# Performance work log

Hardware: AMD Instinct MI355X
Metric: run time of the kernel (lower is better)

Reference implementation:

```python
import jax, jax.numpy as jnp
import numpy as np

HIDDEN = 1024
HEADS = 16
HEAD_DIM = HIDDEN // HEADS


def setup_inputs() -> dict:
    key = jax.random.key(0)
    ks = jax.random.split(key, 11)
    B, S = 2, 2048
    s = 1.0 / np.sqrt(HIDDEN)
    return {
        "query": jax.random.normal(ks[0], (B, S, HIDDEN), jnp.float32),
        "key": jax.random.normal(ks[1], (B, S, HIDDEN), jnp.float32),
        "value": jax.random.normal(ks[2], (B, S, HIDDEN), jnp.float32),
        "Wq": jax.random.normal(ks[3], (HIDDEN, HIDDEN), jnp.float32) * s,
        "bq": jnp.zeros((HIDDEN,), jnp.float32),
        "Wk": jax.random.normal(ks[4], (HIDDEN, HIDDEN), jnp.float32) * s,
        "bk": jnp.zeros((HIDDEN,), jnp.float32),
        "Wv": jax.random.normal(ks[5], (HIDDEN, HIDDEN), jnp.float32) * s,
        "bv": jnp.zeros((HIDDEN,), jnp.float32),
        "Wo": jax.random.normal(ks[6], (HIDDEN, HIDDEN), jnp.float32) * s,
        "bo": jnp.zeros((HIDDEN,), jnp.float32),
    }


def reference(query, key, value, Wq, bq, Wk, bk, Wv, bv, Wo, bo):
    B, S, _ = query.shape
    # QKV projections (torch Linear: x @ W.T + b)
    Q = query @ Wq.T + bq
    K = key @ Wk.T + bk
    V = value @ Wv.T + bv
    # split heads: [B, S, H, D] -> [B, H, S, D]
    Q = Q.reshape(B, S, HEADS, HEAD_DIM).transpose(0, 2, 1, 3)
    K = K.reshape(B, S, HEADS, HEAD_DIM).transpose(0, 2, 1, 3)
    V = V.reshape(B, S, HEADS, HEAD_DIM).transpose(0, 2, 1, 3)
    scale = jnp.sqrt(jnp.float32(HEAD_DIM))
    # energy = Q K^T / sqrt(d)  -> [B, H, Sq, Sk]
    energy = jnp.einsum("bhqd,bhkd->bhqk", Q, K) / scale
    attn = jax.nn.softmax(energy, axis=-1)
    # dropout p=0.0 in eval -> identity
    x = jnp.einsum("bhqk,bhkd->bhqd", attn, V)
    x = x.transpose(0, 2, 1, 3).reshape(B, S, HIDDEN)
    return x @ Wo.T + bo
```

## Files before the change

kernel.cpp:

```cpp
#include <hip/hip_runtime.h>

typedef __attribute__((ext_vector_type(8))) short short8;
typedef __attribute__((ext_vector_type(4))) float f32x4;

#define SEQ 2048
#define NB 2
#define HID 1024
#define NH 16
#define HD 64
#define MS (NB * SEQ)

#define QSCALE 0.18033688011112042f

typedef const __attribute__((address_space(1))) unsigned int* gptr_t;
typedef __attribute__((address_space(3))) unsigned int* lptr_t;

__device__ inline ushort f2bf(float f) {
  union { float f; unsigned u; } x; x.f = f;
  unsigned r = x.u + 0x7fffu + ((x.u >> 16) & 1u);
  return (ushort)(r >> 16);
}

__device__ inline unsigned cvt_pk_bf16(float lo, float hi) {
  unsigned r;
  asm volatile("v_cvt_pk_bf16_f32 %0, %1, %2" : "=v"(r) : "v"(lo), "v"(hi));
  return r;
}

__global__ void cast3(const float* __restrict__ a, const float* __restrict__ b,
                      const float* __restrict__ c, ushort* __restrict__ oa,
                      ushort* __restrict__ ob, ushort* __restrict__ oc, int n4) {
  const int z = blockIdx.y;
  const float* in = (z == 0) ? a : (z == 1) ? b : c;
  ushort* out = (z == 0) ? oa : (z == 1) ? ob : oc;
  int i = blockIdx.x * 256 + threadIdx.x;
  if (i >= n4) return;
  float4 v = reinterpret_cast<const float4*>(in)[i];
  ushort4 o;
  o.x = f2bf(v.x); o.y = f2bf(v.y); o.z = f2bf(v.z); o.w = f2bf(v.w);
  reinterpret_cast<ushort4*>(out)[i] = o;
}

__global__ void cast4(const float* __restrict__ a, const float* __restrict__ b,
                      const float* __restrict__ c, const float* __restrict__ d,
                      ushort* __restrict__ oa, ushort* __restrict__ ob,
                      ushort* __restrict__ oc, ushort* __restrict__ od, int n4) {
  const int z = blockIdx.y;
  const float* in = (z == 0) ? a : (z == 1) ? b : (z == 2) ? c : d;
  ushort* out = (z == 0) ? oa : (z == 1) ? ob : (z == 2) ? oc : od;
  int i = blockIdx.x * 256 + threadIdx.x;
  if (i >= n4) return;
  float4 v = reinterpret_cast<const float4*>(in)[i];
  ushort4 o;
  o.x = f2bf(v.x); o.y = f2bf(v.y); o.z = f2bf(v.z); o.w = f2bf(v.w);
  reinterpret_cast<ushort4*>(out)[i] = o;
}

template <int BN, int OUT>
__device__ __forceinline__ void gemm_body(const ushort* __restrict__ A,
                                          const ushort* __restrict__ B,
                                          const float* __restrict__ bias,
                                          void* __restrict__ Out,
                                          ushort* As, ushort* Bs) {
  constexpr int NJ = BN / 32;
  const int tid = threadIdx.x;
  const int wave = tid >> 6, lane = tid & 63;
  const int lr = lane & 15, lg = lane >> 4;
  const int wr = wave >> 1, wc = wave & 1;
  const int bm = blockIdx.y, bn = blockIdx.x;

  f32x4 acc[4][NJ];
#pragma unroll
  for (int i = 0; i < 4; ++i)
#pragma unroll
    for (int j = 0; j < NJ; ++j) acc[i][j] = (f32x4)(0.f);

  const int l4 = lane >> 2;
  const int lc = (lane & 3) * 8;

  for (int k0 = 0; k0 < HID; k0 += 32) {
#pragma unroll
    for (int c = 0; c < 2; ++c) {
      const int chunk = wave * 2 + c;
      const ushort* ga = &A[(size_t)(bm * 128 + chunk * 16 + l4) * HID + k0 + lc];
      __builtin_amdgcn_global_load_lds((gptr_t)(const void*)ga, (lptr_t)(void*)&As[chunk * 512], 16, 0, 0);
    }
    if (BN == 128) {
#pragma unroll
      for (int c = 0; c < 2; ++c) {
        const int chunk = wave * 2 + c;
        const ushort* gb = &B[(size_t)(bn * BN + chunk * 16 + l4) * HID + k0 + lc];
        __builtin_amdgcn_global_load_lds((gptr_t)(const void*)gb, (lptr_t)(void*)&Bs[chunk * 512], 16, 0, 0);
      }
    } else {
      const ushort* gb = &B[(size_t)(bn * BN + wave * 16 + l4) * HID + k0 + lc];
      __builtin_amdgcn_global_load_lds((gptr_t)(const void*)gb, (lptr_t)(void*)&Bs[wave * 512], 16, 0, 0);
    }
    __syncthreads();
    short8 af[4], bf[NJ];
#pragma unroll
    for (int i = 0; i < 4; ++i)
      af[i] = *reinterpret_cast<const short8*>(&As[(wr * 64 + i * 16 + lr) * 32 + lg * 8]);
#pragma unroll
    for (int j = 0; j < NJ; ++j)
      bf[j] = *reinterpret_cast<const short8*>(&Bs[(wc * (BN / 2) + j * 16 + lr) * 32 + lg * 8]);
#pragma unroll
    for (int i = 0; i < 4; ++i)
#pragma unroll
      for (int j = 0; j < NJ; ++j)
        acc[i][j] = __builtin_amdgcn_mfma_f32_16x16x32_bf16(af[i], bf[j], acc[i][j], 0, 0, 0);
    __syncthreads();
  }

#pragma unroll
  for (int i = 0; i < 4; ++i)
#pragma unroll
    for (int j = 0; j < NJ; ++j) {
      const int row0 = bm * 128 + wr * 64 + i * 16 + lg * 4;
      const int col = bn * BN + wc * (BN / 2) + j * 16 + lr;
      const float bv = bias[col];
      if (OUT == 0) {
#pragma unroll
        for (int r = 0; r < 4; ++r)
          ((float*)Out)[(size_t)(row0 + r) * HID + col] = acc[i][j][r] + bv;
      } else if (OUT == 1) {
#pragma unroll
        for (int r = 0; r < 4; ++r)
          ((ushort*)Out)[(size_t)(row0 + r) * HID + col] = f2bf(acc[i][j][r] + bv);
      } else if (OUT == 2) {
#pragma unroll
        for (int r = 0; r < 4; ++r)
          ((ushort*)Out)[(size_t)(row0 + r) * HID + col] = f2bf((acc[i][j][r] + bv) * QSCALE);
      } else {
        uint2 w;
        w.x = cvt_pk_bf16(acc[i][j][0] + bv, acc[i][j][1] + bv);
        w.y = cvt_pk_bf16(acc[i][j][2] + bv, acc[i][j][3] + bv);
        size_t off = ((size_t)((row0 >> 11) * NH + (col >> 6)) << 17) +
                     ((size_t)(col & 63) << 11) + (size_t)(row0 & 2047);
        *reinterpret_cast<uint2*>(&((ushort*)Out)[off]) = w;
      }
    }
}

__global__ __launch_bounds__(256) void gemm_qkv(const ushort* __restrict__ A0, const ushort* __restrict__ A1,
                                                const ushort* __restrict__ A2, const ushort* __restrict__ W0,
                                                const ushort* __restrict__ W1, const ushort* __restrict__ W2,
                                                const float* __restrict__ b0, const float* __restrict__ b1,
                                                const float* __restrict__ b2, ushort* __restrict__ O0,
                                                ushort* __restrict__ O1, ushort* __restrict__ O2) {
  __shared__ alignas(16) ushort As[128 * 32];
  __shared__ alignas(16) ushort Bs[128 * 32];
  const int z = blockIdx.z;
  if (z == 0)      gemm_body<128, 2>(A0, W0, b0, O0, As, Bs);
  else if (z == 1) gemm_body<128, 1>(A1, W1, b1, O1, As, Bs);
  else             gemm_body<128, 3>(A2, W2, b2, O2, As, Bs);
}

__global__ __launch_bounds__(256) void gemm_wo(const ushort* __restrict__ A, const ushort* __restrict__ W,
                                               const float* __restrict__ bias, float* __restrict__ O) {
  __shared__ alignas(16) ushort As[128 * 32];
  __shared__ alignas(16) ushort Bs[64 * 32];
  gemm_body<64, 0>(A, W, bias, O, As, Bs);
}

__global__ __launch_bounds__(256) void attn_kernel(const ushort* __restrict__ Q,
                                                   const ushort* __restrict__ Kp,
                                                   const ushort* __restrict__ VT,
                                                   ushort* __restrict__ Op) {
  __shared__ alignas(16) ushort Ks[2 * 4096];
  __shared__ alignas(16) ushort Vs[2 * 4096];

  const int qt = blockIdx.x;
  const int bh = blockIdx.y;
  const int b = bh >> 4, h = bh & 15;
  const int tid = threadIdx.x;
  const int wave = tid >> 6;
  const int lane = tid & 63;
  const int lr = lane & 15;
  const int lg = lane >> 4;

  const size_t base = (size_t)b * SEQ * HID + h * HD;
  const size_t vtbase = (size_t)bh * HD * SEQ;

  short8 qf[2];
  const int qrow = qt * 64 + wave * 16 + lr;
#pragma unroll
  for (int kk = 0; kk < 2; ++kk)
    qf[kk] = *reinterpret_cast<const short8*>(&Q[base + (size_t)qrow * HID + kk * 32 + lg * 8]);

  f32x4 acc[4];
#pragma unroll
  for (int nd = 0; nd < 4; ++nd) acc[nd] = (f32x4)(0.f);
  float mrun = -1e30f, lrun = 0.f;

  const int rsub = lane >> 3;
  const int srcsl = ((lane & 7) ^ rsub) * 8;
  const int s0 = lr + ((lg & 1) << 5);
  const int s1v = s0 + 16;

  auto stage = [&](int buf, int kt) {
#pragma unroll
    for (int c = 0; c < 2; ++c) {
      const int chunk = wave * 2 + c;
      const int row = chunk * 8 + rsub;
      const ushort* gk = &Kp[base + (size_t)(kt * 64 + row) * HID + srcsl];
      __builtin_amdgcn_global_load_lds((gptr_t)(const void*)gk,
                                       (lptr_t)(void*)&Ks[buf * 4096 + chunk * 512], 16, 0, 0);
      const ushort* gv = &VT[vtbase + (size_t)row * SEQ + kt * 64 + srcsl];
      __builtin_amdgcn_global_load_lds((gptr_t)(const void*)gv,
                                       (lptr_t)(void*)&Vs[buf * 4096 + chunk * 512], 16, 0, 0);
    }
  };

  stage(0, 0);
  __syncthreads();

  int cur = 0;
  for (int kt = 0; kt < SEQ / 64; ++kt) {
    const int nxt = (kt + 1 < SEQ / 64) ? kt + 1 : 0;
    stage(cur ^ 1, nxt);

    const char* kb = (const char*)&Ks[cur * 4096];
    const char* vb = (const char*)&Vs[cur * 4096];

    f32x4 sa[4];
#pragma unroll
    for (int n = 0; n < 4; ++n) sa[n] = (f32x4)(0.f);
#pragma unroll
    for (int kk = 0; kk < 2; ++kk) {
      short8 kf[4];
#pragma unroll
      for (int n = 0; n < 4; ++n)
        kf[n] = *reinterpret_cast<const short8*>(
            kb + (n * 16 + lr) * 128 + ((kk * 64 + lg * 16) ^ ((lr & 7) << 4)));
#pragma unroll
      for (int n = 0; n < 4; ++n)
        sa[n] = __builtin_amdgcn_mfma_f32_16x16x32_bf16(kf[n], qf[kk], sa[n], 0, 0, 0);
    }

    float pmax = sa[0][0];
#pragma unroll
    for (int n = 0; n < 4; ++n)
#pragma unroll
      for (int r = 0; r < 4; ++r) pmax = fmaxf(pmax, sa[n][r]);
    pmax = fmaxf(pmax, __shfl_xor(pmax, 16, 64));
    pmax = fmaxf(pmax, __shfl_xor(pmax, 32, 64));
    if (__any(pmax > mrun + 8.f)) {
      const float mnew = fmaxf(mrun, pmax);
      const float corr = exp2f(mrun - mnew);
      mrun = mnew;
      lrun *= corr;
#pragma unroll
      for (int nd = 0; nd < 4; ++nd) acc[nd] *= corr;
    }
    float psum = 0.f;
#pragma unroll
    for (int n = 0; n < 4; ++n)
#pragma unroll
      for (int r = 0; r < 4; ++r) {
        float p = exp2f(sa[n][r] - mrun);
        sa[n][r] = p;
        psum += p;
      }
    psum += __shfl_xor(psum, 16, 64);
    psum += __shfl_xor(psum, 32, 64);
    lrun += psum;

    short8 vtf[4][2];
#pragma unroll
    for (int nd = 0; nd < 4; ++nd)
#pragma unroll
      for (int kk = 0; kk < 2; ++kk)
        vtf[nd][kk] = *reinterpret_cast<const short8*>(
            vb + (nd * 16 + lr) * 128 + ((kk * 64 + lg * 16) ^ ((lr & 7) << 4)));

#pragma unroll
    for (int kk = 0; kk < 2; ++kk) {
      unsigned pw0 = 0, pw1 = 0, pw2 = 0, pw3 = 0;
#pragma unroll
      for (int half = 0; half < 2; ++half) {
        const int nsel = kk * 2 + half;
        unsigned w0 = cvt_pk_bf16(sa[nsel][0], sa[nsel][1]);
        unsigned w1 = cvt_pk_bf16(sa[nsel][2], sa[nsel][3]);
        int d0 = __shfl((int)w0, s0, 64);
        int d1 = __shfl((int)w1, s0, 64);
        int d2 = __shfl((int)w0, s1v, 64);
        int d3 = __shfl((int)w1, s1v, 64);
        const bool take = ((lg >> 1) == half);
        pw0 = take ? (unsigned)d0 : pw0;
        pw1 = take ? (unsigned)d1 : pw1;
        pw2 = take ? (unsigned)d2 : pw2;
        pw3 = take ? (unsigned)d3 : pw3;
      }
      union { unsigned u[4]; short8 v; } pu;
      pu.u[0] = pw0; pu.u[1] = pw1; pu.u[2] = pw2; pu.u[3] = pw3;
#pragma unroll
      for (int nd = 0; nd < 4; ++nd)
        acc[nd] = __builtin_amdgcn_mfma_f32_16x16x32_bf16(vtf[nd][kk], pu.v, acc[nd], 0, 0, 0);
    }
    __syncthreads();
    cur ^= 1;
  }

  const float linv = 1.f / lrun;
#pragma unroll
  for (int nd = 0; nd < 4; ++nd) {
    uint2 o;
    o.x = cvt_pk_bf16(acc[nd][0] * linv, acc[nd][1] * linv);
    o.y = cvt_pk_bf16(acc[nd][2] * linv, acc[nd][3] * linv);
    *reinterpret_cast<uint2*>(&Op[base + (size_t)qrow * HID + nd * 16 + lg * 4]) = o;
  }
}

extern "C" void kernel_launch(void* const* d_in, const int* in_sizes, int n_in,
                              void* d_out, int out_size, void* d_ws, size_t ws_size,
                              hipStream_t stream) {
  const float* query = (const float*)d_in[0];
  const float* key   = (const float*)d_in[1];
  const float* value = (const float*)d_in[2];
  const float* Wq = (const float*)d_in[3];
  const float* bq = (const float*)d_in[4];
  const float* Wk = (const float*)d_in[5];
  const float* bk = (const float*)d_in[6];
  const float* Wv = (const float*)d_in[7];
  const float* bv = (const float*)d_in[8];
  const float* Wo = (const float*)d_in[9];
  const float* bo = (const float*)d_in[10];

  const size_t actElems = (size_t)MS * HID;
  const size_t wElems = (size_t)HID * HID;
  char* ws = (char*)d_ws;
  ushort* qb = (ushort*)(ws + 0);
  ushort* kb = (ushort*)(ws + actElems * 2);
  ushort* vb = (ushort*)(ws + actElems * 4);
  ushort* wq = (ushort*)(ws + actElems * 6);
  ushort* wk = (ushort*)(ws + actElems * 6 + wElems * 2);
  ushort* wv = (ushort*)(ws + actElems * 6 + wElems * 4);
  ushort* wo = (ushort*)(ws + actElems * 6 + wElems * 6);
  ushort* Qp   = (ushort*)(ws + actElems * 6 + wElems * 8);
  ushort* Kp   = (ushort*)(ws + actElems * 8 + wElems * 8);
  ushort* VTp  = (ushort*)(ws + actElems * 10 + wElems * 8);
  ushort* attn = (ushort*)(ws + actElems * 12 + wElems * 8);

  dim3 cg3((unsigned)(actElems / 4 / 256), 3);
  cast3<<<cg3, 256, 0, stream>>>(query, key, value, qb, kb, vb, (int)(actElems / 4));
  dim3 cg4((unsigned)(wElems / 4 / 256), 4);
  cast4<<<cg4, 256, 0, stream>>>(Wq, Wk, Wv, Wo, wq, wk, wv, wo, (int)(wElems / 4));

  dim3 gq(HID / 128, MS / 128, 3);
  gemm_qkv<<<gq, 256, 0, stream>>>(qb, kb, vb, wq, wk, wv, bq, bk, bv, Qp, Kp, VTp);

  dim3 ga(SEQ / 64, NB * NH);
  attn_kernel<<<ga, 256, 0, stream>>>(Qp, Kp, VTp, attn);

  dim3 go(HID / 64, MS / 128);
  gemm_wo<<<go, 256, 0, stream>>>(attn, wo, bo, (float*)d_out);
}
```

Before: 295.5 us.

## Rewrite attention with 32x32 MFMA, split-KV waves, and separate V transpose

The attention kernel now uses 512-thread blocks covering 128 query rows each. Two wave groups each process half of the key sequence, using 32x32x16 MFMA tiles and a larger shared-memory buffer, and their partial softmax states are merged through LDS at the end. The V projection GEMM now writes row-major output, and a separate transpose kernel builds V^T instead of the scattered transposed store in the GEMM epilogue. This is meant to raise MFMA efficiency and reuse of K/V tiles per block. The costs are an extra kernel launch, an extra pass over V, and more LDS per block, which may limit occupancy.

```diff
diff --git a/kernel.cpp b/kernel.cpp
--- a/kernel.cpp
+++ b/kernel.cpp
@@ -2,6 +2,7 @@
 
 typedef __attribute__((ext_vector_type(8))) short short8;
 typedef __attribute__((ext_vector_type(4))) float f32x4;
+typedef __attribute__((ext_vector_type(16))) float f32x16;
 
 #define SEQ 2048
 #define NB 2
@@ -21,9 +22,9 @@
   return (ushort)(r >> 16);
 }
 
-__device__ inline unsigned cvt_pk_bf16(float lo, float hi) {
+__device__ __forceinline__ unsigned cvt_pk_bf16(float lo, float hi) {
   unsigned r;
-  asm volatile("v_cvt_pk_bf16_f32 %0, %1, %2" : "=v"(r) : "v"(lo), "v"(hi));
+  asm("v_cvt_pk_bf16_f32 %0, %1, %2" : "=v"(r) : "v"(lo), "v"(hi));
   return r;
 }
 
@@ -119,25 +120,15 @@
       const int row0 = bm * 128 + wr * 64 + i * 16 + lg * 4;
       const int col = bn * BN + wc * (BN / 2) + j * 16 + lr;
       const float bv = bias[col];
-      if (OUT == 0) {
-#pragma unroll
-        for (int r = 0; r < 4; ++r)
-          ((float*)Out)[(size_t)(row0 + r) * HID + col] = acc[i][j][r] + bv;
-      } else if (OUT == 1) {
-#pragma unroll
-        for (int r = 0; r < 4; ++r)
-          ((ushort*)Out)[(size_t)(row0 + r) * HID + col] = f2bf(acc[i][j][r] + bv);
-      } else if (OUT == 2) {
-#pragma unroll
-        for (int r = 0; r < 4; ++r)
-          ((ushort*)Out)[(size_t)(row0 + r) * HID + col] = f2bf((acc[i][j][r] + bv) * QSCALE);
-      } else {
-        uint2 w;
-        w.x = cvt_pk_bf16(acc[i][j][0] + bv, acc[i][j][1] + bv);
-        w.y = cvt_pk_bf16(acc[i][j][2] + bv, acc[i][j][3] + bv);
-        size_t off = ((size_t)((row0 >> 11) * NH + (col >> 6)) << 17) +
-                     ((size_t)(col & 63) << 11) + (size_t)(row0 & 2047);
-        *reinterpret_cast<uint2*>(&((ushort*)Out)[off]) = w;
+#pragma unroll
+      for (int r = 0; r < 4; ++r) {
+        float v = acc[i][j][r] + bv;
+        if (OUT == 0)
+          ((float*)Out)[(size_t)(row0 + r) * HID + col] = v;
+        else if (OUT == 1)
+          ((ushort*)Out)[(size_t)(row0 + r) * HID + col] = f2bf(v);
+        else
+          ((ushort*)Out)[(size_t)(row0 + r) * HID + col] = f2bf(v * QSCALE);
       }
     }
 }
@@ -153,7 +144,7 @@
   const int z = blockIdx.z;
   if (z == 0)      gemm_body<128, 2>(A0, W0, b0, O0, As, Bs);
   else if (z == 1) gemm_body<128, 1>(A1, W1, b1, O1, As, Bs);
-  else             gemm_body<128, 3>(A2, W2, b2, O2, As, Bs);
+  else             gemm_body<128, 1>(A2, W2, b2, O2, As, Bs);
 }
 
 __global__ __launch_bounds__(256) void gemm_wo(const ushort* __restrict__ A, const ushort* __restrict__ W,
@@ -163,152 +154,231 @@
   gemm_body<64, 0>(A, W, bias, O, As, Bs);
 }
 
-__global__ __launch_bounds__(256) void attn_kernel(const ushort* __restrict__ Q,
-                                                   const ushort* __restrict__ Kp,
-                                                   const ushort* __restrict__ VT,
-                                                   ushort* __restrict__ Op) {
-  __shared__ alignas(16) ushort Ks[2 * 4096];
-  __shared__ alignas(16) ushort Vs[2 * 4096];
-
-  const int qt = blockIdx.x;
-  const int bh = blockIdx.y;
+__global__ __launch_bounds__(256) void vt_kernel(const ushort* __restrict__ Vp, ushort* __restrict__ VT) {
+  __shared__ ushort Lt[64][68];
+  const int sb = blockIdx.x, bh = blockIdx.y;
   const int b = bh >> 4, h = bh & 15;
+  const int t = threadIdx.x;
+  const int s4 = (t & 15) * 4, d4 = (t >> 4) * 4;
+  ushort v[4][4];
+#pragma unroll
+  for (int r = 0; r < 4; ++r) {
+    ushort4 x = *reinterpret_cast<const ushort4*>(
+        &Vp[(size_t)(b * SEQ + sb * 64 + s4 + r) * HID + h * 64 + d4]);
+    v[r][0] = x.x; v[r][1] = x.y; v[r][2] = x.z; v[r][3] = x.w;
+  }
+#pragma unroll
+  for (int j = 0; j < 4; ++j) {
+    ushort4 y; y.x = v[0][j]; y.y = v[1][j]; y.z = v[2][j]; y.w = v[3][j];
+    *reinterpret_cast<ushort4*>(&Lt[d4 + j][s4]) = y;
+  }
+  __syncthreads();
+  const int dl = t >> 2, s0 = (t & 3) * 16;
+  ushort4 o[4];
+#pragma unroll
+  for (int p = 0; p < 4; ++p) o[p] = *reinterpret_cast<const ushort4*>(&Lt[dl][s0 + p * 4]);
+  ushort* dst = &VT[((size_t)bh * HD + dl) * SEQ + sb * 64 + s0];
+#pragma unroll
+  for (int p = 0; p < 4; ++p) *reinterpret_cast<ushort4*>(&dst[p * 4]) = o[p];
+}
+
+__device__ __forceinline__ short8 ldfrag(const char* tb, int r, int g) {
+  return *reinterpret_cast<const short8*>(tb + r * 128 + ((g * 16) ^ ((r & 7) << 4)));
+}
+
+__global__ __launch_bounds__(512, 4) void attn_kernel(const ushort* __restrict__ Q,
+                                                      const ushort* __restrict__ Kp,
+                                                      const ushort* __restrict__ VT,
+                                                      ushort* __restrict__ Op) {
+  __shared__ alignas(16) ushort lds[32768];
+
+  const int bh = blockIdx.x;
+  const int b = bh >> 4, h = bh & 15;
+  const int qt = blockIdx.y;
   const int tid = threadIdx.x;
-  const int wave = tid >> 6;
-  const int lane = tid & 63;
-  const int lr = lane & 15;
-  const int lg = lane >> 4;
+  const int w = tid >> 6, lane = tid & 63;
+  const int q = lane & 31, hi = lane >> 5;
+  const int qsub = w & 3, chf = w >> 2;
 
   const size_t base = (size_t)b * SEQ * HID + h * HD;
   const size_t vtbase = (size_t)bh * HD * SEQ;
 
-  short8 qf[2];
-  const int qrow = qt * 64 + wave * 16 + lr;
-#pragma unroll
-  for (int kk = 0; kk < 2; ++kk)
-    qf[kk] = *reinterpret_cast<const short8*>(&Q[base + (size_t)qrow * HID + kk * 32 + lg * 8]);
-
-  f32x4 acc[4];
-#pragma unroll
-  for (int nd = 0; nd < 4; ++nd) acc[nd] = (f32x4)(0.f);
-  float mrun = -1e30f, lrun = 0.f;
-
-  const int rsub = lane >> 3;
-  const int srcsl = ((lane & 7) ^ rsub) * 8;
-  const int s0 = lr + ((lg & 1) << 5);
-  const int s1v = s0 + 16;
-
-  auto stage = [&](int buf, int kt) {
-#pragma unroll
-    for (int c = 0; c < 2; ++c) {
-      const int chunk = wave * 2 + c;
-      const int row = chunk * 8 + rsub;
-      const ushort* gk = &Kp[base + (size_t)(kt * 64 + row) * HID + srcsl];
-      __builtin_amdgcn_global_load_lds((gptr_t)(const void*)gk,
-                                       (lptr_t)(void*)&Ks[buf * 4096 + chunk * 512], 16, 0, 0);
-      const ushort* gv = &VT[vtbase + (size_t)row * SEQ + kt * 64 + srcsl];
-      __builtin_amdgcn_global_load_lds((gptr_t)(const void*)gv,
-                                       (lptr_t)(void*)&Vs[buf * 4096 + chunk * 512], 16, 0, 0);
-    }
+  const int qrow = qt * 128 + qsub * 32 + q;
+  short8 qf[4];
+#pragma unroll
+  for (int s = 0; s < 4; ++s)
+    qf[s] = *reinterpret_cast<const short8*>(&Q[base + (size_t)qrow * HID + s * 16 + hi * 8]);
+
+  f32x16 acc0 = (f32x16)(0.f), acc1 = (f32x16)(0.f);
+  float mrun = -3e38f;
+  float ps0 = 0.f, ps1 = 0.f, ps2 = 0.f, ps3 = 0.f;
+
+  const int tsel = w >> 1, part = w & 1, sh = tsel & 1;
+  const bool isK = tsel < 2;
+  const int r8 = lane >> 3;
+  const int sx = ((lane & 7) ^ r8) * 8;
+
+  auto stage = [&](int buf, int ktb) {
+    const int kt = ktb + sh * 16;
+#pragma unroll
+    for (int c = 0; c < 4; ++c) {
+      const int G = part * 4 + c, r = G * 8 + r8;
+      const ushort* src;
+      ushort* dst;
+      if (isK) {
+        src = &Kp[base + (size_t)(kt * 64 + r) * HID + sx];
+        dst = &lds[(sh * 2 + buf) * 4096 + G * 512];
+      } else {
+        src = &VT[vtbase + (size_t)r * SEQ + kt * 64 + sx];
+        dst = &lds[16384 + (sh * 2 + buf) * 4096 + G * 512];
+      }
+      __builtin_amdgcn_global_load_lds((gptr_t)(const void*)src, (lptr_t)(void*)dst, 16, 0, 0);
+    }
+  };
+
+  auto mkfrag = [&](const unsigned* Wg) -> short8 {
+    unsigned X0 = (unsigned)__shfl_xor((int)Wg[0], 32, 64);
+    unsigned X1 = (unsigned)__shfl_xor((int)Wg[1], 32, 64);
+    unsigned X2 = (unsigned)__shfl_xor((int)Wg[2], 32, 64);
+    unsigned X3 = (unsigned)__shfl_xor((int)Wg[3], 32, 64);
+    union { unsigned u[4]; short8 v; } p;
+    p.u[0] = hi ? X2 : Wg[0];
+    p.u[1] = hi ? X3 : Wg[1];
+    p.u[2] = hi ? Wg[2] : X0;
+    p.u[3] = hi ? Wg[3] : X1;
+    return p.v;
   };
 
   stage(0, 0);
   __syncthreads();
 
-  int cur = 0;
-  for (int kt = 0; kt < SEQ / 64; ++kt) {
-    const int nxt = (kt + 1 < SEQ / 64) ? kt + 1 : 0;
-    stage(cur ^ 1, nxt);
-
-    const char* kb = (const char*)&Ks[cur * 4096];
-    const char* vb = (const char*)&Vs[cur * 4096];
-
-    f32x4 sa[4];
-#pragma unroll
-    for (int n = 0; n < 4; ++n) sa[n] = (f32x4)(0.f);
-#pragma unroll
-    for (int kk = 0; kk < 2; ++kk) {
-      short8 kf[4];
-#pragma unroll
-      for (int n = 0; n < 4; ++n)
-        kf[n] = *reinterpret_cast<const short8*>(
-            kb + (n * 16 + lr) * 128 + ((kk * 64 + lg * 16) ^ ((lr & 7) << 4)));
-#pragma unroll
-      for (int n = 0; n < 4; ++n)
-        sa[n] = __builtin_amdgcn_mfma_f32_16x16x32_bf16(kf[n], qf[kk], sa[n], 0, 0, 0);
-    }
-
-    float pmax = sa[0][0];
-#pragma unroll
-    for (int n = 0; n < 4; ++n)
-#pragma unroll
-      for (int r = 0; r < 4; ++r) pmax = fmaxf(pmax, sa[n][r]);
-    pmax = fmaxf(pmax, __shfl_xor(pmax, 16, 64));
-    pmax = fmaxf(pmax, __shfl_xor(pmax, 32, 64));
-    if (__any(pmax > mrun + 8.f)) {
-      const float mnew = fmaxf(mrun, pmax);
-      const float corr = exp2f(mrun - mnew);
+  int buf = 0;
+  for (int ktb = 0; ktb < 16; ++ktb) {
+    stage(buf ^ 1, (ktb + 1) & 15);
+
+    const char* kb = (const char*)lds + (chf * 2 + buf) * 8192;
+    const char* vb = (const char*)lds + 32768 + (chf * 2 + buf) * 8192;
+
+    f32x16 s0 = (f32x16)(0.f), s1 = (f32x16)(0.f);
+#pragma unroll
+    for (int cs = 0; cs < 4; ++cs) {
+      short8 a = ldfrag(kb, q, cs * 2 + hi);
+      s0 = __builtin_amdgcn_mfma_f32_32x32x16_bf16(a, qf[cs], s0, 0, 0, 0);
+    }
+#pragma unroll
+    for (int cs = 0; cs < 4; ++cs) {
+      short8 a = ldfrag(kb, 32 + q, cs * 2 + hi);
+      s1 = __builtin_amdgcn_mfma_f32_32x32x16_bf16(a, qf[cs], s1, 0, 0, 0);
+    }
+
+    float t8[8];
+#pragma unroll
+    for (int i = 0; i < 8; ++i)
+      t8[i] = fmaxf(fmaxf(s0[i], s0[i + 8]), fmaxf(s1[i], s1[i + 8]));
+    float pm = fmaxf(fmaxf(fmaxf(t8[0], t8[4]), fmaxf(t8[1], t8[5])),
+                     fmaxf(fmaxf(t8[2], t8[6]), fmaxf(t8[3], t8[7])));
+    pm = fmaxf(pm, __shfl_xor(pm, 32, 64));
+    if (__any(pm > mrun + 8.f)) {
+      const float mnew = fmaxf(mrun, pm);
+      const float corr = __builtin_amdgcn_exp2f(mrun - mnew);
       mrun = mnew;
-      lrun *= corr;
-#pragma unroll
-      for (int nd = 0; nd < 4; ++nd) acc[nd] *= corr;
-    }
-    float psum = 0.f;
-#pragma unroll
-    for (int n = 0; n < 4; ++n)
-#pragma unroll
-      for (int r = 0; r < 4; ++r) {
-        float p = exp2f(sa[n][r] - mrun);
-        sa[n][r] = p;
-        psum += p;
+      ps0 *= corr; ps1 *= corr; ps2 *= corr; ps3 *= corr;
+#pragma unroll
+      for (int i = 0; i < 16; ++i) { acc0[i] *= corr; acc1[i] *= corr; }
+    }
+#pragma unroll
+    for (int i = 0; i < 16; ++i) {
+      s0[i] = __builtin_amdgcn_exp2f(s0[i] - mrun);
+      s1[i] = __builtin_amdgcn_exp2f(s1[i] - mrun);
+    }
+    float a8[8];
+#pragma unroll
+    for (int i = 0; i < 8; ++i) a8[i] = (s0[i] + s0[i + 8]) + (s1[i] + s1[i + 8]);
+    ps0 += a8[0] + a8[4]; ps1 += a8[1] + a8[5];
+    ps2 += a8[2] + a8[6]; ps3 += a8[3] + a8[7];
+
+    {
+      unsigned W[8];
+#pragma unroll
+      for (int i = 0; i < 8; ++i) W[i] = cvt_pk_bf16(s0[2 * i], s0[2 * i + 1]);
+      short8 p0 = mkfrag(W);
+      short8 p1 = mkfrag(W + 4);
+      short8 vf;
+      vf = ldfrag(vb, q,      0 + hi); acc0 = __builtin_amdgcn_mfma_f32_32x32x16_bf16(vf, p0, acc0, 0, 0, 0);
+      vf = ldfrag(vb, 32 + q, 0 + hi); acc1 = __builtin_amdgcn_mfma_f32_32x32x16_bf16(vf, p0, acc1, 0, 0, 0);
+      vf = ldfrag(vb, q,      2 + hi); acc0 = __builtin_amdgcn_mfma_f32_32x32x16_bf16(vf, p1, acc0, 0, 0, 0);
+      vf = ldfrag(vb, 32 + q, 2 + hi); acc1 = __builtin_amdgcn_mfma_f32_32x32x16_bf16(vf, p1, acc1, 0, 0, 0);
+    }
+    {
+      unsigned W[8];
+#pragma unroll
+      for (int i = 0; i < 8; ++i) W[i] = cvt_pk_bf16(s1[2 * i], s1[2 * i + 1]);
+      short8 p0 = mkfrag(W);
+      short8 p1 = mkfrag(W + 4);
+      short8 vf;
+      vf = ldfrag(vb, q,      4 + hi); acc0 = __builtin_amdgcn_mfma_f32_32x32x16_bf16(vf, p0, acc0, 0, 0, 0);
+      vf = ldfrag(vb, 32 + q, 4 + hi); acc1 = __builtin_amdgcn_mfma_f32_32x32x16_bf16(vf, p0, acc1, 0, 0, 0);
+      vf = ldfrag(vb, q,      6 + hi); acc0 = __builtin_amdgcn_mfma_f32_32x32x16_bf16(vf, p1, acc0, 0, 0, 0);
+      vf = ldfrag(vb, 32 + q, 6 + hi); acc1 = __builtin_amdgcn_mfma_f32_32x32x16_bf16(vf, p1, acc1, 0, 0, 0);
+    }
+    __syncthreads();
+    buf ^= 1;
+  }
+
+  float lsum = (ps0 + ps1) + (ps2 + ps3);
+  const float lfull = lsum + __shfl_xor(lsum, 32, 64);
+
+  __syncthreads();
+  float* fl = (float*)lds;
+  const int p = w & 3;
+  float* ob = fl + p * 2048 + lane * 32;
+  if (w >= 4) {
+#pragma unroll
+    for (int i = 0; i < 4; ++i) {
+      f32x4 x = {acc0[4 * i], acc0[4 * i + 1], acc0[4 * i + 2], acc0[4 * i + 3]};
+      *reinterpret_cast<f32x4*>(ob + 4 * (i ^ (lane & 7))) = x;
+    }
+#pragma unroll
+    for (int i = 0; i < 4; ++i) {
+      f32x4 x = {acc1[4 * i], acc1[4 * i + 1], acc1[4 * i + 2], acc1[4 * i + 3]};
+      *reinterpret_cast<f32x4*>(ob + 4 * ((i + 4) ^ (lane & 7))) = x;
+    }
+    fl[8192 + (p * 64 + lane) * 2] = mrun;
+    fl[8192 + (p * 64 + lane) * 2 + 1] = lfull;
+  }
+  __syncthreads();
+  if (w < 4) {
+    const float m1 = fl[8192 + (p * 64 + lane) * 2];
+    const float l1 = fl[8192 + (p * 64 + lane) * 2 + 1];
+    float o1[32];
+#pragma unroll
+    for (int s = 0; s < 8; ++s) {
+      f32x4 x = *reinterpret_cast<const f32x4*>(ob + 4 * (s ^ (lane & 7)));
+      o1[4 * s] = x[0]; o1[4 * s + 1] = x[1]; o1[4 * s + 2] = x[2]; o1[4 * s + 3] = x[3];
+    }
+    const float mnew = fmaxf(mrun, m1);
+    const float c0 = __builtin_amdgcn_exp2f(mrun - mnew);
+    const float c1 = __builtin_amdgcn_exp2f(m1 - mnew);
+    const float linv = 1.f / (lfull * c0 + l1 * c1);
+#pragma unroll
+    for (int g = 0; g < 4; ++g) {
+      {
+        float x0 = (acc0[4 * g + 0] * c0 + o1[4 * g + 0] * c1) * linv;
+        float x1 = (acc0[4 * g + 1] * c0 + o1[4 * g + 1] * c1) * linv;
+        float x2 = (acc0[4 * g + 2] * c0 + o1[4 * g + 2] * c1) * linv;
+        float x3 = (acc0[4 * g + 3] * c0 + o1[4 * g + 3] * c1) * linv;
+        uint2 wd; wd.x = cvt_pk_bf16(x0, x1); wd.y = cvt_pk_bf16(x2, x3);
+        *reinterpret_cast<uint2*>(&Op[base + (size_t)qrow * HID + g * 8 + hi * 4]) = wd;
       }
-    psum += __shfl_xor(psum, 16, 64);
-    psum += __shfl_xor(psum, 32, 64);
-    lrun += psum;
-
-    short8 vtf[4][2];
-#pragma unroll
-    for (int nd = 0; nd < 4; ++nd)
-#pragma unroll
-      for (int kk = 0; kk < 2; ++kk)
-        vtf[nd][kk] = *reinterpret_cast<const short8*>(
-            vb + (nd * 16 + lr) * 128 + ((kk * 64 + lg * 16) ^ ((lr & 7) << 4)));
-
-#pragma unroll
-    for (int kk = 0; kk < 2; ++kk) {
-      unsigned pw0 = 0, pw1 = 0, pw2 = 0, pw3 = 0;
-#pragma unroll
-      for (int half = 0; half < 2; ++half) {
-        const int nsel = kk * 2 + half;
-        unsigned w0 = cvt_pk_bf16(sa[nsel][0], sa[nsel][1]);
-        unsigned w1 = cvt_pk_bf16(sa[nsel][2], sa[nsel][3]);
-        int d0 = __shfl((int)w0, s0, 64);
-        int d1 = __shfl((int)w1, s0, 64);
-        int d2 = __shfl((int)w0, s1v, 64);
-        int d3 = __shfl((int)w1, s1v, 64);
-        const bool take = ((lg >> 1) == half);
-        pw0 = take ? (unsigned)d0 : pw0;
-        pw1 = take ? (unsigned)d1 : pw1;
-        pw2 = take ? (unsigned)d2 : pw2;
-        pw3 = take ? (unsigned)d3 : pw3;
+      {
+        float x0 = (acc1[4 * g + 0] * c0 + o1[16 + 4 * g + 0] * c1) * linv;
+        float x1 = (acc1[4 * g + 1] * c0 + o1[16 + 4 * g + 1] * c1) * linv;
+        float x2 = (acc1[4 * g + 2] * c0 + o1[16 + 4 * g + 2] * c1) * linv;
+        float x3 = (acc1[4 * g + 3] * c0 + o1[16 + 4 * g + 3] * c1) * linv;
+        uint2 wd; wd.x = cvt_pk_bf16(x0, x1); wd.y = cvt_pk_bf16(x2, x3);
+        *reinterpret_cast<uint2*>(&Op[base + (size_t)qrow * HID + 32 + g * 8 + hi * 4]) = wd;
       }
-      union { unsigned u[4]; short8 v; } pu;
-      pu.u[0] = pw0; pu.u[1] = pw1; pu.u[2] = pw2; pu.u[3] = pw3;
-#pragma unroll
-      for (int nd = 0; nd < 4; ++nd)
-        acc[nd] = __builtin_amdgcn_mfma_f32_16x16x32_bf16(vtf[nd][kk], pu.v, acc[nd], 0, 0, 0);
-    }
-    __syncthreads();
-    cur ^= 1;
-  }
-
-  const float linv = 1.f / lrun;
-#pragma unroll
-  for (int nd = 0; nd < 4; ++nd) {
-    uint2 o;
-    o.x = cvt_pk_bf16(acc[nd][0] * linv, acc[nd][1] * linv);
-    o.y = cvt_pk_bf16(acc[nd][2] * linv, acc[nd][3] * linv);
-    *reinterpret_cast<uint2*>(&Op[base + (size_t)qrow * HID + nd * 16 + lg * 4]) = o;
+    }
   }
 }
 
@@ -340,7 +410,7 @@
   ushort* Qp   = (ushort*)(ws + actElems * 6 + wElems * 8);
   ushort* Kp   = (ushort*)(ws + actElems * 8 + wElems * 8);
   ushort* VTp  = (ushort*)(ws + actElems * 10 + wElems * 8);
-  ushort* attn = (ushort*)(ws + actElems * 12 + wElems * 8);
+  ushort* XB   = (ushort*)(ws + actElems * 12 + wElems * 8);
 
   dim3 cg3((unsigned)(actElems / 4 / 256), 3);
   cast3<<<cg3, 256, 0, stream>>>(query, key, value, qb, kb, vb, (int)(actElems / 4));
@@ -348,11 +418,14 @@
   cast4<<<cg4, 256, 0, stream>>>(Wq, Wk, Wv, Wo, wq, wk, wv, wo, (int)(wElems / 4));
 
   dim3 gq(HID / 128, MS / 128, 3);
-  gemm_qkv<<<gq, 256, 0, stream>>>(qb, kb, vb, wq, wk, wv, bq, bk, bv, Qp, Kp, VTp);
-
-  dim3 ga(SEQ / 64, NB * NH);
-  attn_kernel<<<ga, 256, 0, stream>>>(Qp, Kp, VTp, attn);
+  gemm_qkv<<<gq, 256, 0, stream>>>(qb, kb, vb, wq, wk, wv, bq, bk, bv, Qp, Kp, XB);
+
+  dim3 gv(SEQ / 64, NB * NH);
+  vt_kernel<<<gv, 256, 0, stream>>>(XB, VTp);
+
+  dim3 ga(NB * NH, SEQ / 128);
+  attn_kernel<<<ga, 512, 0, stream>>>(Qp, Kp, VTp, XB);
 
   dim3 go(HID / 64, MS / 128);
-  gemm_wo<<<go, 256, 0, stream>>>(attn, wo, bo, (float*)d_out);
-}
+  gemm_wo<<<go, 256, 0, stream>>>(XB, wo, bo, (float*)d_out);
+}
```

Result: faster. 251.5 us (-14.9%).
